# Performance work log

Hardware: AMD Instinct MI355X
Metric: run time of the kernel (lower is better)

The kernel has to match this reference:

```python
import jax, jax.numpy as jnp
import numpy as np

N, IN_DIM, HID, HEADS = 20000, 3000, 128, 4
S_DIM, P_DIM = 32, 32
E = 320000
NEG_SLOPE = 0.2
ETA = 1e-6


def _glorot(key, shape):
    fan_in, fan_out = shape[0], shape[-1] if len(shape) > 1 else shape[0]
    lim = np.sqrt(6.0 / (fan_in + fan_out))
    return jax.random.uniform(key, shape, jnp.float32, -lim, lim)


def _gat_params(key, in_dim, out_ch, heads, concat):
    k1, k2, k3 = jax.random.split(key, 3)
    Wl = _glorot(k1, (in_dim, heads * out_ch))
    Wr = _glorot(k2, (in_dim, heads * out_ch))
    att = _glorot(k3, (heads, out_ch))
    b = jnp.zeros((heads * out_ch,) if concat else (out_ch,), jnp.float32)
    return Wl, Wr, att, b


def setup_inputs() -> dict:
    key = jax.random.key(0)
    ks = jax.random.split(key, 6)
    x = jax.random.normal(ks[0], (N, IN_DIM), jnp.float32)
    edge_index = jax.random.randint(ks[1], (2, E), 0, N, jnp.int32)
    out = {"x": x, "edge_index": edge_index}
    for name, kk, (ind, oc, h, cc) in [
        ("s1", ks[2], (IN_DIM, HID, HEADS, True)),
        ("s2", ks[3], (HID * HEADS, S_DIM * 2, 1, False)),
        ("p1", ks[4], (IN_DIM, HID, HEADS, True)),
        ("p2", ks[5], (HID * HEADS, P_DIM * 2, 1, False)),
    ]:
        Wl, Wr, att, b = _gat_params(kk, ind, oc, h, cc)
        out[f"Wl_{name}"] = Wl
        out[f"Wr_{name}"] = Wr
        out[f"att_{name}"] = att
        out[f"b_{name}"] = b
    return out


def gatv2(x, src, dst, Wl, Wr, att, b, heads, out_ch, concat):
    n = x.shape[0]
    xl = (x @ Wl).reshape(n, heads, out_ch)  # source transform
    xr = (x @ Wr).reshape(n, heads, out_ch)  # target transform
    m = xl[src]                                           # [E, H, C] messages
    e = jnp.sum(att * jax.nn.leaky_relu(m + xr[dst], NEG_SLOPE), axis=-1)  # [E, H]
    emax = jax.ops.segment_max(e, dst, num_segments=n)    # self-loops -> no empty segments
    ee = jnp.exp(e - emax[dst])
    denom = jax.ops.segment_sum(ee, dst, num_segments=n)
    alpha = ee / denom[dst]                               # segment softmax over incoming edges
    agg = jax.ops.segment_sum(m * alpha[..., None], dst, num_segments=n)  # [N, H, C]
    out = agg.reshape(n, heads * out_ch) if concat else agg.mean(axis=1)
    return out + b


def reference(x, edge_index, Wl_s1, Wr_s1, att_s1, b_s1, Wl_s2, Wr_s2, att_s2, b_s2,
              Wl_p1, Wr_p1, att_p1, b_p1, Wl_p2, Wr_p2, att_p2, b_p2):
    n = x.shape[0]
    loop = jnp.arange(n, dtype=edge_index.dtype)
    src = jnp.concatenate([edge_index[0], loop])  # add_self_loops (PyG default)
    dst = jnp.concatenate([edge_index[1], loop])
    s = jax.nn.relu(gatv2(x, src, dst, Wl_s1, Wr_s1, att_s1, b_s1, HEADS, HID, True))
    s = gatv2(s, src, dst, Wl_s2, Wr_s2, att_s2, b_s2, 1, S_DIM * 2, False)
    p = gatv2(x, src, dst, Wl_p1, Wr_p1, att_p1, b_p1, HEADS, HID, True)
    p = gatv2(p, src, dst, Wl_p2, Wr_p2, att_p2, b_p2, 1, P_DIM * 2, False)
    mu = jnp.concatenate([s[:, :S_DIM], p[:, :P_DIM]], axis=-1)
    sig = jnp.concatenate([jax.nn.softplus(s[:, S_DIM:]) + ETA,
                           jax.nn.softplus(p[:, P_DIM:]) + ETA], axis=-1)
    return mu, sig
```

## Files before the change

kernel.cpp:

```cpp
#include <hip/hip_runtime.h>
#include <cstdint>

#define NN     20000
#define NE     320000
#define ETOT   340000
#define K1R    3000
#define K1     3072
#define NPAD   20224
#define NCOL1  2048
#define LDA2   1024
#define MU_SZ  1280000

typedef __bf16 bf16x8 __attribute__((ext_vector_type(8)));
typedef float f32x4 __attribute__((ext_vector_type(4)));
typedef unsigned short u16x8 __attribute__((ext_vector_type(8)));

__device__ inline unsigned short f2bf(float f) {
  union { float f; unsigned u; } v; v.f = f;
  unsigned r = v.u + 0x7FFFu + ((v.u >> 16) & 1u);
  return (unsigned short)(r >> 16);
}
__device__ inline float bf2f(unsigned short h) {
  union { unsigned u; float f; } v; v.u = ((unsigned)h) << 16;
  return v.f;
}

typedef const __attribute__((address_space(1))) void* gas1_t;
typedef __attribute__((address_space(3))) void* las3_t;
__device__ inline void llds16(const void* g, void* l) {
  __builtin_amdgcn_global_load_lds((gas1_t)(uintptr_t)g,
                                   (las3_t)(uint32_t)(uintptr_t)l, 16, 0, 0);
}


__global__ __launch_bounds__(256)
void k_convert_x(const float* __restrict__ X, unsigned short* __restrict__ Xb) {
  const int CH = K1 / 8;
  int idx = blockIdx.x * 256 + threadIdx.x;
  if (idx >= NPAD * CH) return;
  int r = idx / CH, c8 = (idx % CH) * 8;
  u16x8 o;
  if (r < NN && c8 < K1R) {
    const float4* p = (const float4*)(X + (size_t)r * K1R + c8);
    float4 a = p[0], b = p[1];
    o[0]=f2bf(a.x); o[1]=f2bf(a.y); o[2]=f2bf(a.z); o[3]=f2bf(a.w);
    o[4]=f2bf(b.x); o[5]=f2bf(b.y); o[6]=f2bf(b.z); o[7]=f2bf(b.w);
  } else {
#pragma unroll
    for (int j = 0; j < 8; j++) o[j] = 0;
  }
  *(u16x8*)(Xb + (size_t)r * K1 + c8) = o;
}

__global__ __launch_bounds__(256)
void k_pack_w1(const float* __restrict__ W0, const float* __restrict__ W1,
               const float* __restrict__ W2, const float* __restrict__ W3,
               unsigned short* __restrict__ Wp) {
  __shared__ float tile[64][65];
  int k0 = blockIdx.x * 64, n0 = blockIdx.y * 64;
  int m = n0 >> 9, c0 = n0 & 511;
  const float* W = (m == 0) ? W0 : (m == 1) ? W1 : (m == 2) ? W2 : W3;
  int tx = threadIdx.x & 63, ty = threadIdx.x >> 6;
#pragma unroll
  for (int rep = 0; rep < 16; rep++) {
    int i = ty + rep * 4;
    int k = k0 + i;
    tile[i][tx] = (k < K1R) ? W[(size_t)k * 512 + c0 + tx] : 0.f;
  }
  __syncthreads();
#pragma unroll
  for (int rep = 0; rep < 16; rep++) {
    int i = ty + rep * 4;
    Wp[(size_t)(n0 + i) * K1 + k0 + tx] = f2bf(tile[tx][i]);
  }
}

__global__ __launch_bounds__(256)
void k_pack_w2(const float* __restrict__ Wl, const float* __restrict__ Wr,
               unsigned short* __restrict__ B2) {
  int idx = blockIdx.x * 256 + threadIdx.x;
  if (idx >= 128 * 1024) return;
  int n = idx >> 10, k = idx & 1023, kk = k & 511;
  float v = (n < 64) ? Wl[(size_t)kk * 64 + n] : Wr[(size_t)kk * 64 + (n - 64)];
  B2[idx] = f2bf(v);
}


__global__ __launch_bounds__(256)
void k_count(const int* __restrict__ ei, int* __restrict__ counts) {
  int e = blockIdx.x * 256 + threadIdx.x;
  if (e >= ETOT) return;
  int dst = (e < NE) ? ei[NE + e] : (e - NE);
  atomicAdd(&counts[dst], 1);
}

__global__ void k_scan(const int* __restrict__ counts, int* __restrict__ row_ptr) {
  __shared__ int part[1024];
  int t = threadIdx.x;
  int base = t * 20;
  int loc[20];
  int s = 0;
#pragma unroll
  for (int i = 0; i < 20; i++) {
    int idx = base + i;
    loc[i] = s;
    s += (idx < NN) ? counts[idx] : 0;
  }
  part[t] = s;
  __syncthreads();
  for (int off = 1; off < 1024; off <<= 1) {
    int v = (t >= off) ? part[t - off] : 0;
    __syncthreads();
    part[t] += v;
    __syncthreads();
  }
  int pre = (t > 0) ? part[t - 1] : 0;
#pragma unroll
  for (int i = 0; i < 20; i++) {
    int idx = base + i;
    if (idx <= NN) row_ptr[idx] = pre + loc[i];
  }
}

__global__ __launch_bounds__(256)
void k_scatter(const int* __restrict__ ei, const int* __restrict__ row_ptr,
               int* __restrict__ fill, int* __restrict__ csr_src) {
  int e = blockIdx.x * 256 + threadIdx.x;
  if (e >= ETOT) return;
  int s_, d_;
  if (e < NE) { s_ = ei[e]; d_ = ei[NE + e]; } else { s_ = d_ = e - NE; }
  int pos = row_ptr[d_] + atomicAdd(&fill[d_], 1);
  csr_src[pos] = s_;
}


#define NT1 48

#define STAGE_ONE do { \
  if (sctr < 4 * NT1) { \
    int ts_ = sctr >> 2, u_ = sctr & 3, sb_ = ts_ & 1; \
    const unsigned short* gb_; char* lb_; int rb_; \
    if (u_ == 0)      { gb_ = A; rb_ = bmBase + 128; lb_ = lds + (sb_*2+1)*16384; } \
    else if (u_ == 1) { gb_ = B; rb_ = bnBase + 128; lb_ = lds + 65536 + (sb_*2+1)*16384; } \
    else if (u_ == 2) { gb_ = B; rb_ = bnBase;       lb_ = lds + 65536 + (sb_*2+0)*16384; } \
    else              { gb_ = A; rb_ = bmBase;       lb_ = lds + (sb_*2+0)*16384; } \
    const unsigned short* g0_ = gb_ + (size_t)(rb_ + trow) * 3072 + ts_ * 64 + scol; \
    llds16(g0_, lb_ + wid * 1024); \
    llds16(g0_ + (size_t)64 * 3072, lb_ + 8192 + wid * 1024); \
    sctr++; \
  } \
} while (0)

#define RDA(DST, BASE) do { \
  _Pragma("unroll") \
  for (int mi = 0; mi < 2; mi++) { \
    int r_ = rw * 32 + mi * 16 + l15; \
    DST[0][mi] = *(const bf16x8*)((BASE) + r_ * 128 + sw0); \
    DST[1][mi] = *(const bf16x8*)((BASE) + r_ * 128 + sw1); \
  } \
} while (0)

#define RDB(DST, BASE) do { \
  _Pragma("unroll") \
  for (int ni = 0; ni < 4; ni++) { \
    int r_ = cw * 64 + ni * 16 + l15; \
    DST[0][ni] = *(const bf16x8*)((BASE) + r_ * 128 + sw0); \
    DST[1][ni] = *(const bf16x8*)((BASE) + r_ * 128 + sw1); \
  } \
} while (0)

#define MF(MH, NH, AV, BV) do { \
  __builtin_amdgcn_s_setprio(1); \
  _Pragma("unroll") \
  for (int mi = 0; mi < 2; mi++) \
    _Pragma("unroll") \
    for (int ni = 0; ni < 4; ni++) { \
      acc[MH][NH][mi][ni] = __builtin_amdgcn_mfma_f32_16x16x32_bf16(AV[0][mi], BV[0][ni], acc[MH][NH][mi][ni], 0, 0, 0); \
      acc[MH][NH][mi][ni] = __builtin_amdgcn_mfma_f32_16x16x32_bf16(AV[1][mi], BV[1][ni], acc[MH][NH][mi][ni], 0, 0, 0); \
    } \
  __builtin_amdgcn_s_setprio(0); \
} while (0)

__global__ __launch_bounds__(512, 2)
void gemm256(const unsigned short* __restrict__ A, const unsigned short* __restrict__ B,
             unsigned short* __restrict__ C) {
  __shared__ char lds[131072];
  int tid = threadIdx.x, wid = tid >> 6, lane = tid & 63;
  int l15 = lane & 15;
  int rw = wid & 3, cw = wid >> 2;
  int role = (wid >> 2) & 1;
  int bid = blockIdx.x;
  int bn = bid & 7, bm = bid >> 3;
  int bmBase = bm * 256, bnBase = bn * 256;
  int trow = tid >> 3;
  int scol = ((tid & 7) ^ ((tid >> 3) & 7)) * 8;
  int sw0 = (((lane >> 4) + 0) ^ (lane & 7)) * 16;
  int sw1 = (((lane >> 4) + 4) ^ (lane & 7)) * 16;
  f32x4 acc[2][2][2][4] = {};

  int sctr = 0;
  for (int i = 0; i < 4; i++) STAGE_ONE;
  asm volatile("s_waitcnt vmcnt(0)" ::: "memory");
  __builtin_amdgcn_s_barrier();
  asm volatile("" ::: "memory");

  for (int t = 0; t < NT1; t++) {
    int buf = t & 1;
    const char* A0h = lds + (buf * 2 + 0) * 16384;
    const char* A1h = lds + (buf * 2 + 1) * 16384;
    const char* B0h = lds + 65536 + (buf * 2 + 0) * 16384;
    const char* B1h = lds + 65536 + (buf * 2 + 1) * 16384;
    bf16x8 a0[2][2], a1[2][2], b0[2][4], b1[2][4];

    if (role == 0) {
      STAGE_ONE;
      RDA(a0, A0h); RDB(b0, B0h);
      MF(0, 0, a0, b0);
      STAGE_ONE;
      RDA(a1, A1h);
      MF(1, 0, a1, b0);
      STAGE_ONE;
      RDB(b1, B1h);
      MF(1, 1, a1, b1);
      STAGE_ONE;
      MF(0, 1, a0, b1);
    } else {
      STAGE_ONE;
      RDA(a1, A1h); RDB(b1, B1h);
      MF(1, 1, a1, b1);
      STAGE_ONE;
      RDA(a0, A0h);
      MF(0, 1, a0, b1);
      STAGE_ONE;
      RDB(b0, B0h);
      MF(0, 0, a0, b0);
      STAGE_ONE;
      MF(1, 0, a1, b0);
    }
    asm volatile("s_waitcnt vmcnt(0)" ::: "memory");
    __builtin_amdgcn_s_barrier();
    asm volatile("" ::: "memory");
  }

  unsigned short (*sq)[128] = (unsigned short (*)[128])lds;
#pragma unroll
  for (int mh = 0; mh < 2; mh++)
#pragma unroll
    for (int nh = 0; nh < 2; nh++) {
      __syncthreads();
#pragma unroll
      for (int mi = 0; mi < 2; mi++)
#pragma unroll
        for (int ni = 0; ni < 4; ni++)
#pragma unroll
          for (int r = 0; r < 4; r++)
            sq[rw * 32 + mi * 16 + (lane >> 4) * 4 + r][cw * 64 + ni * 16 + l15] =
                f2bf(acc[mh][nh][mi][ni][r]);
      __syncthreads();
#pragma unroll
      for (int it = 0; it < 4; it++) {
        int idx = it * 512 + tid;
        int row = idx >> 4, ch = idx & 15;
        *(u16x8*)(C + (size_t)(bmBase + mh * 128 + row) * NCOL1 + bnBase + nh * 128 + ch * 8) =
            *(const u16x8*)&sq[row][ch * 8];
      }
    }
}


__global__ __launch_bounds__(256)
void gemm_l2(const unsigned short* __restrict__ As, const unsigned short* __restrict__ Bs,
             float* __restrict__ Cs,
             const unsigned short* __restrict__ Ap, const unsigned short* __restrict__ Bp,
             float* __restrict__ Cp) {
  const int K = LDA2, lda = LDA2, ldb = LDA2, ldc = 128, mreal = NN;
  const unsigned short* A = blockIdx.y ? Ap : As;
  const unsigned short* B = blockIdx.y ? Bp : Bs;
  float* C = blockIdx.y ? Cp : Cs;
  __shared__ char smem_raw[16384];
  unsigned short* sA = (unsigned short*)smem_raw;
  unsigned short* sB = sA + 128 * 32;
  int bm = blockIdx.x;
  int tid = threadIdx.x, wid = tid >> 6, lane = tid & 63;
  int wr = wid >> 1, wc = wid & 1;
  f32x4 acc[4][4] = {};

  int ar = 32 * wid + (lane >> 2);
  int acol = (lane & 3) * 8;
  const unsigned short* Ag = A + (size_t)(bm * 128 + ar) * lda + acol;
  const unsigned short* Bg = B + (size_t)ar * ldb + acol;
  unsigned short* la0 = sA + (wid * 2) * 512;
  unsigned short* lb0 = sB + (wid * 2) * 512;
  int frow = lane & 15, koff = (lane >> 4) * 8;

  for (int kt = 0; kt < K; kt += 32) {
    llds16(Ag + kt, la0);
    llds16(Ag + kt + (size_t)16 * lda, la0 + 512);
    llds16(Bg + kt, lb0);
    llds16(Bg + kt + (size_t)16 * ldb, lb0 + 512);
    __syncthreads();
    bf16x8 af[4], bfr[4];
#pragma unroll
    for (int mi = 0; mi < 4; mi++)
      af[mi] = *(const bf16x8*)(sA + (wr * 64 + mi * 16 + frow) * 32 + koff);
#pragma unroll
    for (int ni = 0; ni < 4; ni++)
      bfr[ni] = *(const bf16x8*)(sB + (wc * 64 + ni * 16 + frow) * 32 + koff);
#pragma unroll
    for (int mi = 0; mi < 4; mi++)
#pragma unroll
      for (int ni = 0; ni < 4; ni++)
        acc[mi][ni] = __builtin_amdgcn_mfma_f32_16x16x32_bf16(af[mi], bfr[ni], acc[mi][ni], 0, 0, 0);
    __syncthreads();
  }

#pragma unroll
  for (int mi = 0; mi < 4; mi++) {
    int grow0 = bm * 128 + wr * 64 + mi * 16 + (lane >> 4) * 4;
#pragma unroll
    for (int ni = 0; ni < 4; ni++) {
      int gcol = wc * 64 + ni * 16 + (lane & 15);
#pragma unroll
      for (int r = 0; r < 4; r++) {
        int grow = grow0 + r;
        if (grow < mreal) C[(size_t)grow * ldc + gcol] = acc[mi][ni][r];
      }
    }
  }
}


__global__ __launch_bounds__(256)
void edge_agg1(const unsigned short* __restrict__ XL1,
               const int* __restrict__ row_ptr, const int* __restrict__ csr_src,
               const float* __restrict__ att_s, const float* __restrict__ att_p,
               const float* __restrict__ b_s, const float* __restrict__ b_p,
               unsigned short* __restrict__ A2s, unsigned short* __restrict__ A2p) {
  int gw = (blockIdx.x * 256 + threadIdx.x) >> 6;
  if (gw >= NN * 2) return;
  int n = gw >> 1, br = gw & 1;
  int lane = threadIdx.x & 63;
  int cb = lane * 8;
  const float* att = br ? att_p : att_s;
  const float* bias = br ? b_p : b_s;
  float xr[8], at[8], agg[8];
  bf16x8 xrv = *(const bf16x8*)(XL1 + (size_t)n * NCOL1 + br * 1024 + 512 + cb);
#pragma unroll
  for (int j = 0; j < 8; j++) { xr[j] = (float)xrv[j]; at[j] = att[cb + j]; agg[j] = 0.f; }
  float M = -1e30f, S = 0.f;
  const size_t srcoff = (size_t)br * 1024 + cb;
  int pe = row_ptr[n + 1];
  for (int p = row_ptr[n]; p < pe; ++p) {
    int src = csr_src[p];
    bf16x8 mv = *(const bf16x8*)(XL1 + (size_t)src * NCOL1 + srcoff);
    float mj[8], part = 0.f;
#pragma unroll
    for (int j = 0; j < 8; j++) {
      mj[j] = (float)mv[j];
      float t = mj[j] + xr[j];
      t = (t > 0.f) ? t : 0.2f * t;
      part = fmaf(at[j], t, part);
    }
#pragma unroll
    for (int w = 1; w < 16; w <<= 1) part += __shfl_xor(part, w);
    float nm = fmaxf(M, part);
    float fac = __expf(M - nm);
    float wgt = __expf(part - nm);
    S = S * fac + wgt;
#pragma unroll
    for (int j = 0; j < 8; j++) agg[j] = agg[j] * fac + wgt * mj[j];
    M = nm;
  }
  float inv = 1.f / S;
  u16x8 hv, lv;
  unsigned short* A2 = br ? A2p : A2s;
#pragma unroll
  for (int j = 0; j < 8; j++) {
    float v = agg[j] * inv + bias[cb + j];
    if (!br) v = fmaxf(v, 0.f);
    unsigned short h = f2bf(v);
    float lo = v - bf2f(h);
    hv[j] = h; lv[j] = f2bf(lo);
  }
  *(u16x8*)(A2 + (size_t)n * LDA2 + cb) = hv;
  *(u16x8*)(A2 + (size_t)n * LDA2 + 512 + cb) = lv;
}


__global__ __launch_bounds__(256)
void edge_agg2(const float* __restrict__ C2s, const float* __restrict__ C2p,
               const int* __restrict__ row_ptr, const int* __restrict__ csr_src,
               const float* __restrict__ att_s, const float* __restrict__ att_p,
               const float* __restrict__ b_s, const float* __restrict__ b_p,
               float* __restrict__ out) {
  int gw = (blockIdx.x * 256 + threadIdx.x) >> 6;
  if (gw >= NN * 2) return;
  int n = gw >> 1, br = gw & 1;
  int lane = threadIdx.x & 63;
  const float* C2 = br ? C2p : C2s;
  float xr = C2[(size_t)n * 128 + 64 + lane];
  float at = (br ? att_p : att_s)[lane];
  float M = -1e30f, S = 0.f, agg = 0.f;
  int pe = row_ptr[n + 1];
  for (int p = row_ptr[n]; p < pe; ++p) {
    int src = csr_src[p];
    float m = C2[(size_t)src * 128 + lane];
    float t = m + xr;
    t = (t > 0.f) ? t : 0.2f * t;
    float part = at * t;
#pragma unroll
    for (int w = 1; w < 64; w <<= 1) part += __shfl_xor(part, w);
    float nm = fmaxf(M, part);
    float fac = __expf(M - nm);
    float wgt = __expf(part - nm);
    S = S * fac + wgt;
    agg = agg * fac + wgt * m;
    M = nm;
  }
  float v = agg / S + (br ? b_p : b_s)[lane];
  if (lane < 32) {
    out[(size_t)n * 64 + br * 32 + lane] = v;
  } else {
    float sp = fmaxf(v, 0.f) + log1pf(__expf(-fabsf(v))) + 1e-6f;
    out[(size_t)MU_SZ + n * 64 + br * 32 + (lane - 32)] = sp;
  }
}


extern "C" void kernel_launch(void* const* d_in, const int* in_sizes, int n_in,
                              void* d_out, int out_size, void* d_ws, size_t ws_size,
                              hipStream_t stream) {
  const float* x      = (const float*)d_in[0];
  const int*   ei     = (const int*)d_in[1];
  const float* Wl_s1  = (const float*)d_in[2];
  const float* Wr_s1  = (const float*)d_in[3];
  const float* att_s1 = (const float*)d_in[4];
  const float* b_s1   = (const float*)d_in[5];
  const float* Wl_s2  = (const float*)d_in[6];
  const float* Wr_s2  = (const float*)d_in[7];
  const float* att_s2 = (const float*)d_in[8];
  const float* b_s2   = (const float*)d_in[9];
  const float* Wl_p1  = (const float*)d_in[10];
  const float* Wr_p1  = (const float*)d_in[11];
  const float* att_p1 = (const float*)d_in[12];
  const float* b_p1   = (const float*)d_in[13];
  const float* Wl_p2  = (const float*)d_in[14];
  const float* Wr_p2  = (const float*)d_in[15];
  const float* att_p2 = (const float*)d_in[16];
  const float* b_p2   = (const float*)d_in[17];

  char* ws = (char*)d_ws;
  unsigned short* Xb   = (unsigned short*)(ws + 0);
  unsigned short* A2s  = (unsigned short*)(ws + 0);
  unsigned short* A2p  = (unsigned short*)(ws + 41156608);
  float*          C2s  = (float*)(ws + 82313216);
  float*          C2p  = (float*)(ws + 92553216);
  unsigned short* B2s  = (unsigned short*)(ws + 102793216);
  unsigned short* B2p  = (unsigned short*)(ws + 103055360);
  unsigned short* Wp   = (unsigned short*)(ws + 124256256);
  unsigned short* XL1  = (unsigned short*)(ws + 136839168);
  int* counts  = (int*)(ws + 219676672);
  int* fill    = (int*)(ws + 219756672);
  int* row_ptr = (int*)(ws + 219836672);
  int* csr_src = (int*)(ws + 219916688);

  hipMemsetAsync(counts, 0, NN * sizeof(int), stream);
  hipMemsetAsync(fill, 0, NN * sizeof(int), stream);

  k_convert_x<<<30336, 256, 0, stream>>>(x, Xb);
  k_pack_w1<<<dim3(48, 32), 256, 0, stream>>>(Wl_s1, Wr_s1, Wl_p1, Wr_p1, Wp);
  k_count<<<(ETOT + 255) / 256, 256, 0, stream>>>(ei, counts);
  k_scan<<<1, 1024, 0, stream>>>(counts, row_ptr);
  k_scatter<<<(ETOT + 255) / 256, 256, 0, stream>>>(ei, row_ptr, fill, csr_src);

  gemm256<<<632, 512, 0, stream>>>(Xb, Wp, XL1);

  k_pack_w2<<<512, 256, 0, stream>>>(Wl_s2, Wr_s2, B2s);
  k_pack_w2<<<512, 256, 0, stream>>>(Wl_p2, Wr_p2, B2p);

  edge_agg1<<<10000, 256, 0, stream>>>(XL1, row_ptr, csr_src, att_s1, att_p1, b_s1, b_p1, A2s, A2p);

  gemm_l2<<<dim3(157, 2), 256, 0, stream>>>(A2s, B2s, C2s, A2p, B2p, C2p);

  edge_agg2<<<10000, 256, 0, stream>>>(C2s, C2p, row_ptr, csr_src, att_s2, att_p2, b_s2, b_p2, (float*)d_out);
}
```

Baseline: 627.7 us.

## Process both GAT branches per wavefront in edge aggregation with source prefetch

```diff
diff --git a/kernel.cpp b/kernel.cpp
--- a/kernel.cpp
+++ b/kernel.cpp
@@ -76,10 +76,14 @@
 }
 
 __global__ __launch_bounds__(256)
-void k_pack_w2(const float* __restrict__ Wl, const float* __restrict__ Wr,
-               unsigned short* __restrict__ B2) {
-  int idx = blockIdx.x * 256 + threadIdx.x;
-  if (idx >= 128 * 1024) return;
+void k_pack_w2b(const float* __restrict__ Wl_s, const float* __restrict__ Wr_s,
+                const float* __restrict__ Wl_p, const float* __restrict__ Wr_p,
+                unsigned short* __restrict__ B2s, unsigned short* __restrict__ B2p) {
+  int gidx = blockIdx.x * 256 + threadIdx.x;
+  int br = gidx >> 17, idx = gidx & 131071;
+  const float* Wl = br ? Wl_p : Wl_s;
+  const float* Wr = br ? Wr_p : Wr_s;
+  unsigned short* B2 = br ? B2p : B2s;
   int n = idx >> 10, k = idx & 1023, kk = k & 511;
   float v = (n < 64) ? Wl[(size_t)kk * 64 + n] : Wr[(size_t)kk * 64 + (n - 64)];
   B2[idx] = f2bf(v);
@@ -336,54 +340,75 @@
                const float* __restrict__ att_s, const float* __restrict__ att_p,
                const float* __restrict__ b_s, const float* __restrict__ b_p,
                unsigned short* __restrict__ A2s, unsigned short* __restrict__ A2p) {
-  int gw = (blockIdx.x * 256 + threadIdx.x) >> 6;
-  if (gw >= NN * 2) return;
-  int n = gw >> 1, br = gw & 1;
+  int n = (blockIdx.x * 256 + threadIdx.x) >> 6;
+  if (n >= NN) return;
   int lane = threadIdx.x & 63;
   int cb = lane * 8;
-  const float* att = br ? att_p : att_s;
-  const float* bias = br ? b_p : b_s;
-  float xr[8], at[8], agg[8];
-  bf16x8 xrv = *(const bf16x8*)(XL1 + (size_t)n * NCOL1 + br * 1024 + 512 + cb);
-#pragma unroll
-  for (int j = 0; j < 8; j++) { xr[j] = (float)xrv[j]; at[j] = att[cb + j]; agg[j] = 0.f; }
-  float M = -1e30f, S = 0.f;
-  const size_t srcoff = (size_t)br * 1024 + cb;
-  int pe = row_ptr[n + 1];
-  for (int p = row_ptr[n]; p < pe; ++p) {
-    int src = csr_src[p];
-    bf16x8 mv = *(const bf16x8*)(XL1 + (size_t)src * NCOL1 + srcoff);
-    float mj[8], part = 0.f;
+  float xs[8], xp[8], as_[8], ap_[8], aggs[8], aggp[8];
+  {
+    bf16x8 xsv = *(const bf16x8*)(XL1 + (size_t)n * NCOL1 + 512 + cb);
+    bf16x8 xpv = *(const bf16x8*)(XL1 + (size_t)n * NCOL1 + 1536 + cb);
+    float4 a0 = *(const float4*)(att_s + cb), a1 = *(const float4*)(att_s + cb + 4);
+    float4 a2 = *(const float4*)(att_p + cb), a3 = *(const float4*)(att_p + cb + 4);
+    as_[0]=a0.x; as_[1]=a0.y; as_[2]=a0.z; as_[3]=a0.w; as_[4]=a1.x; as_[5]=a1.y; as_[6]=a1.z; as_[7]=a1.w;
+    ap_[0]=a2.x; ap_[1]=a2.y; ap_[2]=a2.z; ap_[3]=a2.w; ap_[4]=a3.x; ap_[5]=a3.y; ap_[6]=a3.z; ap_[7]=a3.w;
+#pragma unroll
+    for (int j = 0; j < 8; j++) { xs[j] = (float)xsv[j]; xp[j] = (float)xpv[j]; aggs[j] = 0.f; aggp[j] = 0.f; }
+  }
+  float Ms = -1e30f, Ss = 0.f, Mp = -1e30f, Sp = 0.f;
+  int p0 = row_ptr[n], pe = row_ptr[n + 1];
+  int src = csr_src[p0];
+  bf16x8 ms = *(const bf16x8*)(XL1 + (size_t)src * NCOL1 + cb);
+  bf16x8 mp = *(const bf16x8*)(XL1 + (size_t)src * NCOL1 + 1024 + cb);
+  for (int p = p0; p < pe; ++p) {
+    bf16x8 cs = ms, cp = mp;
+    if (p + 1 < pe) {
+      int s2 = csr_src[p + 1];
+      ms = *(const bf16x8*)(XL1 + (size_t)s2 * NCOL1 + cb);
+      mp = *(const bf16x8*)(XL1 + (size_t)s2 * NCOL1 + 1024 + cb);
+    }
+    float mjs[8], mjp[8], ps_ = 0.f, pp_ = 0.f;
 #pragma unroll
     for (int j = 0; j < 8; j++) {
-      mj[j] = (float)mv[j];
-      float t = mj[j] + xr[j];
+      mjs[j] = (float)cs[j];
+      float t = mjs[j] + xs[j];
       t = (t > 0.f) ? t : 0.2f * t;
-      part = fmaf(at[j], t, part);
-    }
-#pragma unroll
-    for (int w = 1; w < 16; w <<= 1) part += __shfl_xor(part, w);
-    float nm = fmaxf(M, part);
-    float fac = __expf(M - nm);
-    float wgt = __expf(part - nm);
-    S = S * fac + wgt;
-#pragma unroll
-    for (int j = 0; j < 8; j++) agg[j] = agg[j] * fac + wgt * mj[j];
-    M = nm;
-  }
-  float inv = 1.f / S;
-  u16x8 hv, lv;
-  unsigned short* A2 = br ? A2p : A2s;
+      ps_ = fmaf(as_[j], t, ps_);
+      mjp[j] = (float)cp[j];
+      float u = mjp[j] + xp[j];
+      u = (u > 0.f) ? u : 0.2f * u;
+      pp_ = fmaf(ap_[j], u, pp_);
+    }
+#pragma unroll
+    for (int w = 1; w < 16; w <<= 1) { ps_ += __shfl_xor(ps_, w); pp_ += __shfl_xor(pp_, w); }
+    float nms = fmaxf(Ms, ps_);
+    float fs = __expf(Ms - nms), ws_ = __expf(ps_ - nms);
+    Ss = Ss * fs + ws_;
+    float nmp = fmaxf(Mp, pp_);
+    float fp = __expf(Mp - nmp), wp_ = __expf(pp_ - nmp);
+    Sp = Sp * fp + wp_;
+#pragma unroll
+    for (int j = 0; j < 8; j++) {
+      aggs[j] = aggs[j] * fs + ws_ * mjs[j];
+      aggp[j] = aggp[j] * fp + wp_ * mjp[j];
+    }
+    Ms = nms; Mp = nmp;
+  }
+  float invs = 1.f / Ss, invp = 1.f / Sp;
+  u16x8 hs, ls, hp, lp;
 #pragma unroll
   for (int j = 0; j < 8; j++) {
-    float v = agg[j] * inv + bias[cb + j];
-    if (!br) v = fmaxf(v, 0.f);
+    float v = fmaxf(aggs[j] * invs + b_s[cb + j], 0.f);
     unsigned short h = f2bf(v);
-    float lo = v - bf2f(h);
-    hv[j] = h; lv[j] = f2bf(lo);
-  }
-  *(u16x8*)(A2 + (size_t)n * LDA2 + cb) = hv;
-  *(u16x8*)(A2 + (size_t)n * LDA2 + 512 + cb) = lv;
+    hs[j] = h; ls[j] = f2bf(v - bf2f(h));
+    float u = aggp[j] * invp + b_p[cb + j];
+    unsigned short h2 = f2bf(u);
+    hp[j] = h2; lp[j] = f2bf(u - bf2f(h2));
+  }
+  *(u16x8*)(A2s + (size_t)n * LDA2 + cb) = hs;
+  *(u16x8*)(A2s + (size_t)n * LDA2 + 512 + cb) = ls;
+  *(u16x8*)(A2p + (size_t)n * LDA2 + cb) = hp;
+  *(u16x8*)(A2p + (size_t)n * LDA2 + 512 + cb) = lp;
 }
 
 
@@ -393,36 +418,47 @@
                const float* __restrict__ att_s, const float* __restrict__ att_p,
                const float* __restrict__ b_s, const float* __restrict__ b_p,
                float* __restrict__ out) {
-  int gw = (blockIdx.x * 256 + threadIdx.x) >> 6;
-  if (gw >= NN * 2) return;
-  int n = gw >> 1, br = gw & 1;
+  int n = (blockIdx.x * 256 + threadIdx.x) >> 6;
+  if (n >= NN) return;
   int lane = threadIdx.x & 63;
-  const float* C2 = br ? C2p : C2s;
-  float xr = C2[(size_t)n * 128 + 64 + lane];
-  float at = (br ? att_p : att_s)[lane];
-  float M = -1e30f, S = 0.f, agg = 0.f;
-  int pe = row_ptr[n + 1];
-  for (int p = row_ptr[n]; p < pe; ++p) {
-    int src = csr_src[p];
-    float m = C2[(size_t)src * 128 + lane];
-    float t = m + xr;
-    t = (t > 0.f) ? t : 0.2f * t;
-    float part = at * t;
-#pragma unroll
-    for (int w = 1; w < 64; w <<= 1) part += __shfl_xor(part, w);
-    float nm = fmaxf(M, part);
-    float fac = __expf(M - nm);
-    float wgt = __expf(part - nm);
-    S = S * fac + wgt;
-    agg = agg * fac + wgt * m;
-    M = nm;
-  }
-  float v = agg / S + (br ? b_p : b_s)[lane];
+  float xrs = C2s[(size_t)n * 128 + 64 + lane];
+  float xrp = C2p[(size_t)n * 128 + 64 + lane];
+  float ats = att_s[lane], atp = att_p[lane];
+  float Ms = -1e30f, Ss = 0.f, ags = 0.f;
+  float Mp = -1e30f, Sp = 0.f, agp = 0.f;
+  int p0 = row_ptr[n], pe = row_ptr[n + 1];
+  int src = csr_src[p0];
+  float ms = C2s[(size_t)src * 128 + lane];
+  float mp = C2p[(size_t)src * 128 + lane];
+  for (int p = p0; p < pe; ++p) {
+    float cs = ms, cp = mp;
+    if (p + 1 < pe) {
+      int s2 = csr_src[p + 1];
+      ms = C2s[(size_t)s2 * 128 + lane];
+      mp = C2p[(size_t)s2 * 128 + lane];
+    }
+    float t = cs + xrs; t = (t > 0.f) ? t : 0.2f * t;
+    float u = cp + xrp; u = (u > 0.f) ? u : 0.2f * u;
+    float ps_ = ats * t, pp_ = atp * u;
+#pragma unroll
+    for (int w = 1; w < 64; w <<= 1) { ps_ += __shfl_xor(ps_, w); pp_ += __shfl_xor(pp_, w); }
+    float nms = fmaxf(Ms, ps_);
+    float fs = __expf(Ms - nms), ws_ = __expf(ps_ - nms);
+    Ss = Ss * fs + ws_; ags = ags * fs + ws_ * cs; Ms = nms;
+    float nmp = fmaxf(Mp, pp_);
+    float fp = __expf(Mp - nmp), wp_ = __expf(pp_ - nmp);
+    Sp = Sp * fp + wp_; agp = agp * fp + wp_ * cp; Mp = nmp;
+  }
+  float vs = ags / Ss + b_s[lane];
+  float vp = agp / Sp + b_p[lane];
   if (lane < 32) {
-    out[(size_t)n * 64 + br * 32 + lane] = v;
+    out[(size_t)n * 64 + lane] = vs;
+    out[(size_t)n * 64 + 32 + lane] = vp;
   } else {
-    float sp = fmaxf(v, 0.f) + log1pf(__expf(-fabsf(v))) + 1e-6f;
-    out[(size_t)MU_SZ + n * 64 + br * 32 + (lane - 32)] = sp;
+    float sps = fmaxf(vs, 0.f) + log1pf(__expf(-fabsf(vs))) + 1e-6f;
+    float spp = fmaxf(vp, 0.f) + log1pf(__expf(-fabsf(vp))) + 1e-6f;
+    out[(size_t)MU_SZ + n * 64 + (lane - 32)] = sps;
+    out[(size_t)MU_SZ + n * 64 + 32 + (lane - 32)] = spp;
   }
 }
 
@@ -475,12 +511,11 @@
 
   gemm256<<<632, 512, 0, stream>>>(Xb, Wp, XL1);
 
-  k_pack_w2<<<512, 256, 0, stream>>>(Wl_s2, Wr_s2, B2s);
-  k_pack_w2<<<512, 256, 0, stream>>>(Wl_p2, Wr_p2, B2p);
-
-  edge_agg1<<<10000, 256, 0, stream>>>(XL1, row_ptr, csr_src, att_s1, att_p1, b_s1, b_p1, A2s, A2p);
+  k_pack_w2b<<<1024, 256, 0, stream>>>(Wl_s2, Wr_s2, Wl_p2, Wr_p2, B2s, B2p);
+
+  edge_agg1<<<5000, 256, 0, stream>>>(XL1, row_ptr, csr_src, att_s1, att_p1, b_s1, b_p1, A2s, A2p);
 
   gemm_l2<<<dim3(157, 2), 256, 0, stream>>>(A2s, B2s, C2s, A2p, B2p, C2p);
 
-  edge_agg2<<<10000, 256, 0, stream>>>(C2s, C2p, row_ptr, csr_src, att_s2, att_p2, b_s2, b_p2, (float*)d_out);
-}
+  edge_agg2<<<5000, 256, 0, stream>>>(C2s, C2p, row_ptr, csr_src, att_s2, att_p2, b_s2, b_p2, (float*)d_out);
+}
```

New measurement: 613.5 us. -2.3%, faster.
